# Kernel tuning notes

Hardware: AMD Instinct MI355X
Metric: run time of the kernel (lower is better)

Reference implementation:

```python
import jax, jax.numpy as jnp
import numpy as np

STRIDES = (8, 16, 32, 64, 128)
NUM_CONVS = 4
GROUPS = 32
EPS = 1e-5
FEAT_SHAPES = [(8, 256, 100, 152), (8, 256, 50, 76), (8, 256, 25, 38), (8, 256, 13, 19), (8, 256, 7, 10)]


def _conv3x3(x, w, b):
    # x: [B,C,H,W], w: [O,I,3,3] -> SAME padding, stride 1
    y = jax.lax.conv_general_dilated(x, w, (1, 1), 'SAME', dimension_numbers=('NCHW', 'OIHW', 'NCHW'))
    return y + b[None, :, None, None]


def _group_norm(x, g, b):
    B, C, H, W = x.shape
    xr = x.reshape(B, GROUPS, C // GROUPS, H, W)
    m = xr.mean(axis=(2, 3, 4), keepdims=True)
    v = xr.var(axis=(2, 3, 4), keepdims=True)
    xr = (xr - m) * jax.lax.rsqrt(v + EPS)
    return xr.reshape(B, C, H, W) * g[None, :, None, None] + b[None, :, None, None]


def _head(feats, cls_w, cls_b, cls_gn_g, cls_gn_b, box_w, box_b, box_gn_g, box_gn_b,
          logits_w, logits_b, ctr_w, ctr_b, reg_w, reg_b, scales):
    outs = []
    for l, f in enumerate(feats):
        ct, bt = f, f
        for i in range(NUM_CONVS):  # fixed-depth tower loop
            ct = jax.nn.relu(_group_norm(_conv3x3(ct, cls_w[i], cls_b[i]), cls_gn_g[i], cls_gn_b[i]))
            bt = jax.nn.relu(_group_norm(_conv3x3(bt, box_w[i], box_b[i]), box_gn_g[i], box_gn_b[i]))
        logits = _conv3x3(ct, logits_w, logits_b)          # [B,80,H,W]
        ctr = _conv3x3(ct, ctr_w, ctr_b)                   # [B,1,H,W]
        reg = jnp.exp(scales[l] * _conv3x3(bt, reg_w, reg_b))  # [B,4,H,W], torch.exp(Scale(bbox_pred))
        B = f.shape[0]
        outs.append(jnp.concatenate([logits, reg, ctr], axis=1).reshape(B, -1))
    return jnp.concatenate(outs, axis=1)  # [B, sum_l 85*H_l*W_l]


def _locations(feats):
    # FCOS grid locations: (x,y) center of each stride cell, per level, concatenated
    locs = []
    for l, f in enumerate(feats):
        h, w = f.shape[-2:]
        s = STRIDES[l]
        sx = jnp.arange(w, dtype=jnp.float32) * s + s // 2
        sy = jnp.arange(h, dtype=jnp.float32) * s + s // 2
        yy, xx = jnp.meshgrid(sy, sx, indexing='ij')
        locs.append(jnp.stack([xx.reshape(-1), yy.reshape(-1)], axis=1))
    return jnp.concatenate(locs, axis=0)  # [sum HW, 2]


def setup_inputs() -> dict:
    key = jax.random.key(0)
    ks = jax.random.split(key, 12)
    d = {}
    for i, s in enumerate(FEAT_SHAPES):
        d['feat%d' % i] = jax.random.normal(ks[i], s, dtype=jnp.float32)

    def w(k, shape):
        return jax.random.normal(k, shape, dtype=jnp.float32) * 0.01  # init std=0.01

    d['cls_w'] = w(ks[5], (NUM_CONVS, 256, 256, 3, 3))
    d['cls_b'] = jnp.zeros((NUM_CONVS, 256), jnp.float32)
    d['cls_gn_g'] = jnp.ones((NUM_CONVS, 256), jnp.float32)
    d['cls_gn_b'] = jnp.zeros((NUM_CONVS, 256), jnp.float32)
    d['box_w'] = w(ks[6], (NUM_CONVS, 256, 256, 3, 3))
    d['box_b'] = jnp.zeros((NUM_CONVS, 256), jnp.float32)
    d['box_gn_g'] = jnp.ones((NUM_CONVS, 256), jnp.float32)
    d['box_gn_b'] = jnp.zeros((NUM_CONVS, 256), jnp.float32)
    d['logits_w'] = w(ks[7], (80, 256, 3, 3))
    d['logits_b'] = jnp.full((80,), -float(np.log((1.0 - 0.01) / 0.01)), jnp.float32)  # prior_prob bias
    d['ctr_w'] = w(ks[8], (1, 256, 3, 3))
    d['ctr_b'] = jnp.zeros((1,), jnp.float32)
    d['reg_w'] = w(ks[9], (4, 256, 3, 3))
    d['reg_b'] = jnp.zeros((4,), jnp.float32)
    d['scales'] = jnp.ones((5,), jnp.float32)
    return d


def reference(feat0, feat1, feat2, feat3, feat4, cls_w, cls_b, cls_gn_g, cls_gn_b,
              box_w, box_b, box_gn_g, box_gn_b, logits_w, logits_b, ctr_w, ctr_b,
              reg_w, reg_b, scales):
    feats = [feat0, feat1, feat2, feat3, feat4]
    out = _head(feats, cls_w, cls_b, cls_gn_g, cls_gn_b, box_w, box_b, box_gn_g, box_gn_b,
                logits_w, logits_b, ctr_w, ctr_b, reg_w, reg_b, scales)
    locs = _locations(feats)
    return out, locs
```

## Files before the change

kernel.cpp:

```cpp
#include <hip/hip_runtime.h>
#include <hip/hip_bf16.h>

#define TOT85 1722695ULL

using short8 = __attribute__((ext_vector_type(8))) short;
using f32x4  = __attribute__((ext_vector_type(4))) float;

struct Feat5 { const float* p[5]; };

__device__ __forceinline__ float bfbits2f(short u) {
  return __uint_as_float(((unsigned int)(unsigned short)u) << 16);
}
__device__ __forceinline__ short f2bfbits(float f) {
  __hip_bfloat16 h = __float2bfloat16(f);
  return *reinterpret_cast<short*>(&h);
}

#define LVL_TABLES                                                              \
  constexpr int kH[5] = {100, 50, 25, 13, 7};                                   \
  constexpr int kW[5] = {152, 76, 38, 19, 10};                                  \
  constexpr int kNTx[5] = {10, 5, 3, 2, 1};                                     \
  constexpr int kCumT[5] = {0, 130, 165, 177, 181};                             \
  constexpr int kCumHW[5] = {0, 15200, 19000, 19950, 20197};                    \
  constexpr float kInv[5] = {1.f / 121600.f, 1.f / 30400.f, 1.f / 7600.f,       \
                             1.f / 1976.f, 1.f / 560.f};

__global__ __launch_bounds__(256) void repack_k(const float* __restrict__ src,
                                                __hip_bfloat16* __restrict__ dst,
                                                int O, int NOCP, int ocoff) {
  int idx = blockIdx.x * 256 + threadIdx.x;
  if (idx >= O * 2304) return;
  int o = idx / 2304;
  int r = idx - o * 2304;
  int i = r / 9;
  int t = r - i * 9;
  dst[((size_t)(t * 8 + (i >> 5)) * NOCP + (o + ocoff)) * 32 + (i & 31)] =
      __float2bfloat16(src[idx]);
}

__global__ void locations_all_k(float* __restrict__ out) {
  LVL_TABLES
  constexpr int kStride[5] = {8, 16, 32, 64, 128};
  int i = blockIdx.x * 256 + threadIdx.x;
  if (i >= 20267) return;
  int lvl = (i >= 15200) + (i >= 19000) + (i >= 19950) + (i >= 20197);
  int local = i - kCumHW[lvl];
  int W = kW[lvl];
  float s = (float)kStride[lvl];
  int y = local / W, x = local - y * W;
  out[2 * i + 0] = x * s + 0.5f * s;
  out[2 * i + 1] = y * s + 0.5f * s;
}

template <bool NORM_IN, bool SRC_NCHW>
__global__ __launch_bounds__(256, 2) void conv_tower_k(
    Feat5 feats, const __hip_bfloat16* __restrict__ srcb_base,
    const __hip_bfloat16* __restrict__ wpk, const float* __restrict__ bias,
    const float* __restrict__ statsInBase, const float* __restrict__ gamma,
    const float* __restrict__ beta, __hip_bfloat16* __restrict__ dstBase,
    float* __restrict__ statsOutBase) {
  LVL_TABLES
  __shared__ __align__(16) short s_in[180 * 40];
  __shared__ float s_red[64];
  __shared__ float s_a[256], s_c[256];

  const int tid = threadIdx.x;
  const int lane = tid & 63;
  const int wave = tid >> 6;
  const int wm = wave >> 1;
  const int wn = wave & 1;
  const int bx = blockIdx.x;
  const int lvl = (bx >= 130) + (bx >= 165) + (bx >= 177) + (bx >= 181);
  const int H = kH[lvl], W = kW[lvl], nTx = kNTx[lvl];
  const int tloc = bx - kCumT[lvl];
  const int ty = tloc / nTx, tx = tloc - ty * nTx;
  const int x0 = tx * 16, y0 = ty * 8;
  const int b = blockIdx.z;
  const int HW = H * W;
  const size_t lbase = (size_t)2048 * kCumHW[lvl];
  const int l15 = lane & 15;
  const int kg = lane >> 4;
  const int q8 = (tid & 3) * 8;

  if (tid < 64) s_red[tid] = 0.f;
  if (NORM_IN) {
    const float* statsIn = statsInBase + (size_t)lvl * 4096;
    float inv_cnt = kInv[lvl];
    int g = tid >> 3;
    float s = statsIn[(b * 32 + g) * 2 + 0];
    float ss = statsIn[(b * 32 + g) * 2 + 1];
    float m = s * inv_cnt;
    float var = fmaf(-m, m, ss * inv_cnt);
    float rs = rsqrtf(var + 1e-5f);
    float avv = rs * gamma[tid];
    s_a[tid] = avv;
    s_c[tid] = fmaf(-m, avv, beta[tid]);
  }

  f32x4 acc[4][8];
#pragma unroll
  for (int m = 0; m < 4; ++m)
#pragma unroll
    for (int n = 0; n < 8; ++n) acc[m][n] = (f32x4){0.f, 0.f, 0.f, 0.f};

  const short* wlane = (const short*)wpk + ((wn * 128 + l15) * 32 + kg * 8);
  const size_t TAPSTR = (size_t)8 * 256 * 32;

  for (int chunk = 0; chunk < 8; ++chunk) {
    const int ic0 = chunk * 32;
    __syncthreads();
    if (SRC_NCHW) {
      const float* srcf = feats.p[lvl];
      const int pix = tid;
      if (pix < 180) {
        int prow = pix / 18;
        int pcol = pix - prow * 18;
        int gy = y0 + prow - 1, gx = x0 + pcol - 1;
        short8 sv[4];
        bool valid = (gy >= 0 && gy < H && gx >= 0 && gx < W);
        if (valid) {
          const float* p = srcf + (((size_t)(b * 256 + ic0)) * H + gy) * W + gx;
#pragma unroll
          for (int q = 0; q < 4; ++q)
#pragma unroll
            for (int j = 0; j < 8; ++j)
              sv[q][j] = f2bfbits(p[(size_t)(q * 8 + j) * HW]);
        } else {
#pragma unroll
          for (int q = 0; q < 4; ++q) sv[q] = (short8)0;
        }
#pragma unroll
        for (int q = 0; q < 4; ++q) *(short8*)(s_in + pix * 40 + q * 8) = sv[q];
      }
    } else {
      const short* srcb = (const short*)srcb_base + lbase;
      float av[8], cv[8];
#pragma unroll
      for (int j = 0; j < 8; ++j) {
        int c2 = ic0 + q8 + j;
        av[j] = s_a[c2];
        cv[j] = s_c[c2];
      }
      for (int idx = tid; idx < 720; idx += 256) {
        int pix = idx >> 2;
        int prow = pix / 18;
        int pcol = pix - prow * 18;
        int gy = y0 + prow - 1, gx = x0 + pcol - 1;
        short8 o8 = (short8)0;
        if (gy >= 0 && gy < H && gx >= 0 && gx < W) {
          const short* sp = srcb + ((((size_t)b * H + gy) * W + gx) * 256 + ic0 + q8);
          short8 v8 = *(const short8*)sp;
#pragma unroll
          for (int j = 0; j < 8; ++j)
            o8[j] = f2bfbits(fmaxf(fmaf(bfbits2f(v8[j]), av[j], cv[j]), 0.f));
        }
        *(short8*)(s_in + pix * 40 + q8) = o8;
      }
    }
    __syncthreads();

    const short* wch = wlane + (size_t)chunk * 256 * 32;
    short8 bwA[8], bwB[8];
#pragma unroll
    for (int n = 0; n < 8; ++n) bwA[n] = *(const short8*)(wch + n * 512);

    auto tapbody = [&](int tap, short8* curw, short8* nxtw) {
      if (tap < 8) {
        const short* wt = wch + (size_t)(tap + 1) * TAPSTR;
#pragma unroll
        for (int n = 0; n < 8; ++n) nxtw[n] = *(const short8*)(wt + n * 512);
      }
      const int dy = tap / 3, dx = tap - dy * 3;
      short8 af[4];
#pragma unroll
      for (int m = 0; m < 4; ++m)
        af[m] = *(const short8*)(s_in + ((wm * 4 + m + dy) * 18 + (l15 + dx)) * 40 + kg * 8);
#pragma unroll
      for (int m = 0; m < 4; ++m)
#pragma unroll
        for (int n = 0; n < 8; ++n)
          acc[m][n] = __builtin_amdgcn_mfma_f32_16x16x32_bf16(af[m], curw[n], acc[m][n], 0, 0, 0);
    };
#pragma unroll
    for (int tap = 0; tap < 9; tap += 2) {
      tapbody(tap, bwA, bwB);
      if (tap + 1 < 9) tapbody(tap + 1, bwB, bwA);
    }
  }

  short* dst = (short*)dstBase + lbase;
  const int masks[5] = {1, 2, 4, 16, 32};
#pragma unroll
  for (int n = 0; n < 8; ++n) {
    int oc_g = wn * 128 + n * 16 + l15;
    float bv = bias[oc_g];
    float lsum = 0.f, lssq = 0.f;
#pragma unroll
    for (int m = 0; m < 4; ++m) {
      int oy = y0 + wm * 4 + m;
#pragma unroll
      for (int r = 0; r < 4; ++r) {
        int ox = x0 + kg * 4 + r;
        bool valid = (oy < H) && (ox < W);
        float v = acc[m][n][r] + bv;
        if (valid) {
          dst[(((size_t)b * H + oy) * W + ox) * 256 + oc_g] = f2bfbits(v);
          lsum += v;
          lssq += v * v;
        }
      }
    }
#pragma unroll
    for (int s = 0; s < 5; ++s) {
      lsum += __shfl_xor(lsum, masks[s], 64);
      lssq += __shfl_xor(lssq, masks[s], 64);
    }
    if ((lane & 55) == 0) {
      int g2 = ((wn * 8 + n) * 2 + ((lane >> 3) & 1)) * 2;
      atomicAdd(&s_red[g2 + 0], lsum);
      atomicAdd(&s_red[g2 + 1], lssq);
    }
  }
  __syncthreads();
  float* statsOut = statsOutBase + (size_t)lvl * 4096;
  if (tid < 64) atomicAdd(&statsOut[(size_t)b * 64 + tid], s_red[tid]);
}

template <int NREP, int OUT_MODE>
__global__ __launch_bounds__(256, 3) void conv_head_k(
    const __hip_bfloat16* __restrict__ srcb_base, const __hip_bfloat16* __restrict__ wpk,
    const float* __restrict__ bias, const float* __restrict__ bias2,
    const float* __restrict__ statsInBase, const float* __restrict__ gamma,
    const float* __restrict__ beta, float* __restrict__ out,
    const float* __restrict__ scales, int NOCP) {
  LVL_TABLES
  __shared__ __align__(16) short s_in[180 * 40];
  __shared__ float s_a[256], s_c[256];

  const int tid = threadIdx.x;
  const int lane = tid & 63;
  const int wave = tid >> 6;
  const int wm = wave >> 1;
  const int wn = wave & 1;
  const int bx = blockIdx.x;
  const int lvl = (bx >= 130) + (bx >= 165) + (bx >= 177) + (bx >= 181);
  const int H = kH[lvl], W = kW[lvl], nTx = kNTx[lvl];
  const int tloc = bx - kCumT[lvl];
  const int ty = tloc / nTx, tx = tloc - ty * nTx;
  const int x0 = tx * 16, y0 = ty * 8;
  const int b = blockIdx.z;
  const int HW = H * W;
  const size_t lbase = (size_t)2048 * kCumHW[lvl];
  float* out_lvl = out + (size_t)85 * kCumHW[lvl];
  const int l15 = lane & 15;
  const int kg = lane >> 4;
  const int q8 = (tid & 3) * 8;

  {
    const float* statsIn = statsInBase + (size_t)lvl * 4096;
    float inv_cnt = kInv[lvl];
    int g = tid >> 3;
    float s = statsIn[(b * 32 + g) * 2 + 0];
    float ss = statsIn[(b * 32 + g) * 2 + 1];
    float m = s * inv_cnt;
    float var = fmaf(-m, m, ss * inv_cnt);
    float rs = rsqrtf(var + 1e-5f);
    float avv = rs * gamma[tid];
    s_a[tid] = avv;
    s_c[tid] = fmaf(-m, avv, beta[tid]);
  }

  f32x4 acc[4][NREP];
#pragma unroll
  for (int m = 0; m < 4; ++m)
#pragma unroll
    for (int n = 0; n < NREP; ++n) acc[m][n] = (f32x4){0.f, 0.f, 0.f, 0.f};

  const short* wlane = (const short*)wpk + ((wn * NREP * 16 + l15) * 32 + kg * 8);
  const size_t TAPSTR = (size_t)8 * NOCP * 32;

  for (int chunk = 0; chunk < 8; ++chunk) {
    const int ic0 = chunk * 32;
    __syncthreads();
    {
      const short* srcb = (const short*)srcb_base + lbase;
      float av[8], cv[8];
#pragma unroll
      for (int j = 0; j < 8; ++j) {
        int c2 = ic0 + q8 + j;
        av[j] = s_a[c2];
        cv[j] = s_c[c2];
      }
      for (int idx = tid; idx < 720; idx += 256) {
        int pix = idx >> 2;
        int prow = pix / 18;
        int pcol = pix - prow * 18;
        int gy = y0 + prow - 1, gx = x0 + pcol - 1;
        short8 o8 = (short8)0;
        if (gy >= 0 && gy < H && gx >= 0 && gx < W) {
          const short* sp = srcb + ((((size_t)b * H + gy) * W + gx) * 256 + ic0 + q8);
          short8 v8 = *(const short8*)sp;
#pragma unroll
          for (int j = 0; j < 8; ++j)
            o8[j] = f2bfbits(fmaxf(fmaf(bfbits2f(v8[j]), av[j], cv[j]), 0.f));
        }
        *(short8*)(s_in + pix * 40 + q8) = o8;
      }
    }
    __syncthreads();

    const short* wch = wlane + (size_t)chunk * NOCP * 32;
    short8 bwA[NREP], bwB[NREP];
#pragma unroll
    for (int n = 0; n < NREP; ++n) bwA[n] = *(const short8*)(wch + n * 512);

    auto tapbody = [&](int tap, short8* curw, short8* nxtw) {
      if (tap < 8) {
        const short* wt = wch + (size_t)(tap + 1) * TAPSTR;
#pragma unroll
        for (int n = 0; n < NREP; ++n) nxtw[n] = *(const short8*)(wt + n * 512);
      }
      const int dy = tap / 3, dx = tap - dy * 3;
      short8 af[4];
#pragma unroll
      for (int m = 0; m < 4; ++m)
        af[m] = *(const short8*)(s_in + ((wm * 4 + m + dy) * 18 + (l15 + dx)) * 40 + kg * 8);
#pragma unroll
      for (int m = 0; m < 4; ++m)
#pragma unroll
        for (int n = 0; n < NREP; ++n)
          acc[m][n] = __builtin_amdgcn_mfma_f32_16x16x32_bf16(af[m], curw[n], acc[m][n], 0, 0, 0);
    };
#pragma unroll
    for (int tap = 0; tap < 9; tap += 2) {
      tapbody(tap, bwA, bwB);
      if (tap + 1 < 9) tapbody(tap + 1, bwB, bwA);
    }
  }

#pragma unroll
  for (int n = 0; n < NREP; ++n) {
    int oc_l = wn * NREP * 16 + n * 16 + l15;
    int oc_valid = (OUT_MODE == 1) ? 81 : 4;
    float bv;
    if (OUT_MODE == 1)
      bv = (oc_l < 80) ? bias[oc_l] : ((oc_l == 80) ? bias2[0] : 0.f);
    else
      bv = (oc_l < oc_valid) ? bias[oc_l] : 0.f;
#pragma unroll
    for (int m = 0; m < 4; ++m) {
      int oy = y0 + wm * 4 + m;
#pragma unroll
      for (int r = 0; r < 4; ++r) {
        int ox = x0 + kg * 4 + r;
        bool valid = (oy < H) && (ox < W) && (oc_l < oc_valid);
        float v = acc[m][n][r] + bv;
        if (valid) {
          if (OUT_MODE == 1) {
            int och = (oc_l == 80) ? 84 : oc_l;
            out_lvl[(size_t)b * TOT85 + (size_t)och * HW + oy * W + ox] = v;
          } else {
            out_lvl[(size_t)b * TOT85 + (size_t)(80 + oc_l) * HW + oy * W + ox] =
                expf(scales[lvl] * v);
          }
        }
      }
    }
  }
}

extern "C" void kernel_launch(void* const* d_in, const int* in_sizes, int n_in,
                              void* d_out_v, int out_size, void* d_ws, size_t ws_size,
                              hipStream_t stream) {
  (void)in_sizes; (void)n_in; (void)out_size; (void)ws_size;

  Feat5 feats;
  for (int i = 0; i < 5; ++i) feats.p[i] = (const float*)d_in[i];
  Feat5 featsNull;
  for (int i = 0; i < 5; ++i) featsNull.p[i] = nullptr;
  const float* cls_w = (const float*)d_in[5];
  const float* cls_b = (const float*)d_in[6];
  const float* cls_g = (const float*)d_in[7];
  const float* cls_bb = (const float*)d_in[8];
  const float* box_w = (const float*)d_in[9];
  const float* box_b = (const float*)d_in[10];
  const float* box_g = (const float*)d_in[11];
  const float* box_bb = (const float*)d_in[12];
  const float* logits_w = (const float*)d_in[13];
  const float* logits_b = (const float*)d_in[14];
  const float* ctr_w = (const float*)d_in[15];
  const float* ctr_b = (const float*)d_in[16];
  const float* reg_w = (const float*)d_in[17];
  const float* reg_b = (const float*)d_in[18];
  const float* scales = (const float*)d_in[19];
  float* d_out = (float*)d_out_v;

  char* wsp = (char*)d_ws;
  size_t off = 0;
  auto carve = [&](size_t bytes) -> char* {
    char* p = wsp + off;
    off += (bytes + 255) & ~(size_t)255;
    return p;
  };
  const size_t ALLE = (size_t)8 * 20267 * 256;
  __hip_bfloat16* bufA = (__hip_bfloat16*)carve(ALLE * 2);
  __hip_bfloat16* bufB = (__hip_bfloat16*)carve(ALLE * 2);
  const size_t TW = (size_t)9 * 8 * 256 * 32;
  __hip_bfloat16* wpk_cls = (__hip_bfloat16*)carve(4 * TW * 2);
  __hip_bfloat16* wpk_box = (__hip_bfloat16*)carve(4 * TW * 2);
  __hip_bfloat16* wpk_clsh = (__hip_bfloat16*)carve((size_t)9 * 8 * 96 * 32 * 2);
  __hip_bfloat16* wpk_regh = (__hip_bfloat16*)carve((size_t)9 * 8 * 32 * 32 * 2);
  float* stats_all = (float*)carve((size_t)40 * 512 * 4);

  hipMemsetAsync(stats_all, 0, (size_t)40 * 512 * 4, stream);

  auto rp = [&](const float* s, __hip_bfloat16* d, int O, int NOCP, int ocoff) {
    int total = O * 2304;
    hipLaunchKernelGGL(repack_k, dim3((total + 255) / 256), dim3(256), 0, stream, s, d, O, NOCP,
                       ocoff);
  };
  for (int i = 0; i < 4; ++i) {
    rp(cls_w + (size_t)i * 256 * 2304, wpk_cls + (size_t)i * TW, 256, 256, 0);
    rp(box_w + (size_t)i * 256 * 2304, wpk_box + (size_t)i * TW, 256, 256, 0);
  }
  rp(logits_w, wpk_clsh, 80, 96, 0);
  rp(ctr_w, wpk_clsh, 1, 96, 80);
  rp(reg_w, wpk_regh, 4, 32, 0);

  const size_t OUT0 = (size_t)8 * TOT85;
  hipLaunchKernelGGL(locations_all_k, dim3(80), dim3(256), 0, stream, d_out + OUT0);

  dim3 grid(182, 1, 8);
  dim3 blk(256);

  for (int t = 0; t < 2; ++t) {
    const __hip_bfloat16* wpkT = (t == 0) ? wpk_cls : wpk_box;
    const float* bt = (t == 0) ? cls_b : box_b;
    const float* gt = (t == 0) ? cls_g : box_g;
    const float* bbt = (t == 0) ? cls_bb : box_bb;
    auto slot = [&](int i) { return stats_all + (size_t)(t * 4 + i) * 512; };

    hipLaunchKernelGGL((conv_tower_k<false, true>), grid, blk, 0, stream, feats,
                       (const __hip_bfloat16*)nullptr, wpkT, bt, (const float*)nullptr,
                       (const float*)nullptr, (const float*)nullptr, bufA, slot(0));
    __hip_bfloat16* cur = bufA;
    __hip_bfloat16* nxt = bufB;
    for (int i = 1; i < 4; ++i) {
      hipLaunchKernelGGL((conv_tower_k<true, false>), grid, blk, 0, stream, featsNull,
                         (const __hip_bfloat16*)cur, wpkT + (size_t)i * TW, bt + i * 256,
                         slot(i - 1), gt + (i - 1) * 256, bbt + (i - 1) * 256, nxt, slot(i));
      __hip_bfloat16* tmp = cur;
      cur = nxt;
      nxt = tmp;
    }
    if (t == 0) {
      hipLaunchKernelGGL((conv_head_k<3, 1>), grid, blk, 0, stream, (const __hip_bfloat16*)cur,
                         wpk_clsh, logits_b, ctr_b, slot(3), gt + 3 * 256, bbt + 3 * 256,
                         d_out, scales, 96);
    } else {
      hipLaunchKernelGGL((conv_head_k<1, 2>), grid, blk, 0, stream, (const __hip_bfloat16*)cur,
                         wpk_regh, reg_b, (const float*)nullptr, slot(3), gt + 3 * 256,
                         bbt + 3 * 256, d_out, scales, 32);
    }
  }
}
```

Measured before the change: 2.488 ms.

## Widen conv input chunks to 64 channels and prefetch global loads before barrier

The conv tower kernel now stages 64 input channels per shared-memory chunk instead of 32, halving the number of chunk iterations and their barriers. Global loads for the next tile are issued into registers before the __syncthreads, so memory latency can overlap with waves still finishing MFMA work on the previous chunk. The inner loop runs 18 k-steps (9 taps × 2 sub-chunks) with weight double-buffering. This costs more LDS (180×72 shorts) and more registers (fv[32], pv[6]), which may reduce occupancy under launch_bounds(256,2).

```diff
diff --git a/kernel.cpp b/kernel.cpp
--- a/kernel.cpp
+++ b/kernel.cpp
@@ -60,7 +60,7 @@
     const float* __restrict__ beta, __hip_bfloat16* __restrict__ dstBase,
     float* __restrict__ statsOutBase) {
   LVL_TABLES
-  __shared__ __align__(16) short s_in[180 * 40];
+  __shared__ __align__(16) short s_in[180 * 72];
   __shared__ float s_red[64];
   __shared__ float s_a[256], s_c[256];
 
@@ -80,7 +80,7 @@
   const size_t lbase = (size_t)2048 * kCumHW[lvl];
   const int l15 = lane & 15;
   const int kg = lane >> 4;
-  const int q8 = (tid & 3) * 8;
+  const int q8x = (tid & 7) * 8;
 
   if (tid < 64) s_red[tid] = 0.f;
   if (NORM_IN) {
@@ -104,77 +104,119 @@
     for (int n = 0; n < 8; ++n) acc[m][n] = (f32x4){0.f, 0.f, 0.f, 0.f};
 
   const short* wlane = (const short*)wpk + ((wn * 128 + l15) * 32 + kg * 8);
-  const size_t TAPSTR = (size_t)8 * 256 * 32;
-
-  for (int chunk = 0; chunk < 8; ++chunk) {
-    const int ic0 = chunk * 32;
-    __syncthreads();
+
+  const int pixN = tid;
+  int prowN = pixN / 18;
+  int pcolN = pixN - prowN * 18;
+  const int gyN = y0 + prowN - 1, gxN = x0 + pcolN - 1;
+  const bool validN = (pixN < 180) && (gyN >= 0 && gyN < H && gxN >= 0 && gxN < W);
+
+  for (int c = 0; c < 4; ++c) {
+    const int ic0 = c * 64;
+
+    short8 pv[6];
+    float fv[32];
     if (SRC_NCHW) {
       const float* srcf = feats.p[lvl];
-      const int pix = tid;
-      if (pix < 180) {
-        int prow = pix / 18;
-        int pcol = pix - prow * 18;
-        int gy = y0 + prow - 1, gx = x0 + pcol - 1;
-        short8 sv[4];
-        bool valid = (gy >= 0 && gy < H && gx >= 0 && gx < W);
-        if (valid) {
-          const float* p = srcf + (((size_t)(b * 256 + ic0)) * H + gy) * W + gx;
-#pragma unroll
-          for (int q = 0; q < 4; ++q)
-#pragma unroll
-            for (int j = 0; j < 8; ++j)
-              sv[q][j] = f2bfbits(p[(size_t)(q * 8 + j) * HW]);
-        } else {
-#pragma unroll
-          for (int q = 0; q < 4; ++q) sv[q] = (short8)0;
-        }
-#pragma unroll
-        for (int q = 0; q < 4; ++q) *(short8*)(s_in + pix * 40 + q * 8) = sv[q];
+      if (validN) {
+        const float* p = srcf + (((size_t)(b * 256 + ic0)) * H + gyN) * W + gxN;
+#pragma unroll
+        for (int j = 0; j < 32; ++j) fv[j] = p[(size_t)j * HW];
       }
     } else {
       const short* srcb = (const short*)srcb_base + lbase;
+#pragma unroll
+      for (int r = 0; r < 6; ++r) {
+        int idx = r * 256 + tid;
+        pv[r] = (short8)0;
+        if (idx < 1440) {
+          int px = idx >> 3;
+          int prow = px / 18;
+          int pcol = px - prow * 18;
+          int gy = y0 + prow - 1, gx = x0 + pcol - 1;
+          if (gy >= 0 && gy < H && gx >= 0 && gx < W)
+            pv[r] = *(const short8*)(srcb +
+                                     ((((size_t)b * H + gy) * W + gx) * 256 + ic0 + q8x));
+        }
+      }
+    }
+
+    __syncthreads();
+
+    if (SRC_NCHW) {
+      const float* srcf = feats.p[lvl];
+      if (pixN < 180) {
+        short8 sv[4];
+        if (validN) {
+#pragma unroll
+          for (int q = 0; q < 4; ++q)
+#pragma unroll
+            for (int j = 0; j < 8; ++j) sv[q][j] = f2bfbits(fv[q * 8 + j]);
+        } else {
+#pragma unroll
+          for (int q = 0; q < 4; ++q) sv[q] = (short8)0;
+        }
+#pragma unroll
+        for (int q = 0; q < 4; ++q) *(short8*)(s_in + pixN * 72 + q * 8) = sv[q];
+        if (validN) {
+          const float* p = srcf + (((size_t)(b * 256 + ic0 + 32)) * H + gyN) * W + gxN;
+#pragma unroll
+          for (int j = 0; j < 32; ++j) fv[j] = p[(size_t)j * HW];
+#pragma unroll
+          for (int q = 0; q < 4; ++q)
+#pragma unroll
+            for (int j = 0; j < 8; ++j) sv[q][j] = f2bfbits(fv[q * 8 + j]);
+        }
+#pragma unroll
+        for (int q = 0; q < 4; ++q) *(short8*)(s_in + pixN * 72 + 32 + q * 8) = sv[q];
+      }
+    } else {
       float av[8], cv[8];
 #pragma unroll
       for (int j = 0; j < 8; ++j) {
-        int c2 = ic0 + q8 + j;
+        int c2 = ic0 + q8x + j;
         av[j] = s_a[c2];
         cv[j] = s_c[c2];
       }
-      for (int idx = tid; idx < 720; idx += 256) {
-        int pix = idx >> 2;
-        int prow = pix / 18;
-        int pcol = pix - prow * 18;
-        int gy = y0 + prow - 1, gx = x0 + pcol - 1;
-        short8 o8 = (short8)0;
-        if (gy >= 0 && gy < H && gx >= 0 && gx < W) {
-          const short* sp = srcb + ((((size_t)b * H + gy) * W + gx) * 256 + ic0 + q8);
-          short8 v8 = *(const short8*)sp;
-#pragma unroll
-          for (int j = 0; j < 8; ++j)
-            o8[j] = f2bfbits(fmaxf(fmaf(bfbits2f(v8[j]), av[j], cv[j]), 0.f));
-        }
-        *(short8*)(s_in + pix * 40 + q8) = o8;
+#pragma unroll
+      for (int r = 0; r < 6; ++r) {
+        int idx = r * 256 + tid;
+        if (idx < 1440) {
+          int px = idx >> 3;
+          int prow = px / 18;
+          int pcol = px - prow * 18;
+          int gy = y0 + prow - 1, gx = x0 + pcol - 1;
+          short8 o8 = (short8)0;
+          if (gy >= 0 && gy < H && gx >= 0 && gx < W) {
+#pragma unroll
+            for (int j = 0; j < 8; ++j)
+              o8[j] = f2bfbits(fmaxf(fmaf(bfbits2f(pv[r][j]), av[j], cv[j]), 0.f));
+          }
+          *(short8*)(s_in + px * 72 + q8x) = o8;
+        }
       }
     }
     __syncthreads();
 
-    const short* wch = wlane + (size_t)chunk * 256 * 32;
+    const short* wcb = wlane + (size_t)c * 2 * 8192;
     short8 bwA[8], bwB[8];
 #pragma unroll
-    for (int n = 0; n < 8; ++n) bwA[n] = *(const short8*)(wch + n * 512);
-
-    auto tapbody = [&](int tap, short8* curw, short8* nxtw) {
-      if (tap < 8) {
-        const short* wt = wch + (size_t)(tap + 1) * TAPSTR;
+    for (int n = 0; n < 8; ++n) bwA[n] = *(const short8*)(wcb + n * 512);
+
+    auto kbody = [&](int k, short8* curw, short8* nxtw) {
+      if (k < 17) {
+        int kn = k + 1;
+        const short* wt = wcb + ((size_t)((kn >> 1) * 8 + (kn & 1))) * 8192;
 #pragma unroll
         for (int n = 0; n < 8; ++n) nxtw[n] = *(const short8*)(wt + n * 512);
       }
+      const int tap = k >> 1, sub = k & 1;
       const int dy = tap / 3, dx = tap - dy * 3;
       short8 af[4];
 #pragma unroll
       for (int m = 0; m < 4; ++m)
-        af[m] = *(const short8*)(s_in + ((wm * 4 + m + dy) * 18 + (l15 + dx)) * 40 + kg * 8);
+        af[m] = *(const short8*)(s_in + ((wm * 4 + m + dy) * 18 + (l15 + dx)) * 72 +
+                                 sub * 32 + kg * 8);
 #pragma unroll
       for (int m = 0; m < 4; ++m)
 #pragma unroll
@@ -182,9 +224,9 @@
           acc[m][n] = __builtin_amdgcn_mfma_f32_16x16x32_bf16(af[m], curw[n], acc[m][n], 0, 0, 0);
     };
 #pragma unroll
-    for (int tap = 0; tap < 9; tap += 2) {
-      tapbody(tap, bwA, bwB);
-      if (tap + 1 < 9) tapbody(tap + 1, bwB, bwA);
+    for (int k = 0; k < 18; k += 2) {
+      kbody(k, bwA, bwB);
+      kbody(k + 1, bwB, bwA);
     }
   }
 
```

Result: no change. 2.446 ms (-1.7%).

## Stage conv weights in LDS via direct loads and retile tower conv to 32x8x128

Applied to the files above, without the earlier changes.

The tower conv kernel now uses 512-thread blocks covering a 32-wide by 8-tall pixel tile and half of the output channels, with the grid split over output-channel halves. Each 32-channel chunk of the weight panel is copied into shared memory with global_load_lds, replacing per-lane register streaming of weights from global memory, and the padded layout is meant to reduce LDS bank conflicts. Input activations for the next chunk are loaded into registers before the barrier to overlap global latency. The cost is much more LDS per block (about 100KB), which may limit occupancy, and input halos are reloaded once per output-channel half.

```diff
diff --git a/kernel.cpp b/kernel.cpp
--- a/kernel.cpp
+++ b/kernel.cpp
@@ -14,6 +14,11 @@
 __device__ __forceinline__ short f2bfbits(float f) {
   __hip_bfloat16 h = __float2bfloat16(f);
   return *reinterpret_cast<short*>(&h);
+}
+__device__ __forceinline__ void gload_lds16(const void* g, void* l) {
+  __builtin_amdgcn_global_load_lds(
+      (const __attribute__((address_space(1))) unsigned int*)g,
+      (__attribute__((address_space(3))) unsigned int*)l, 16, 0, 0);
 }
 
 #define LVL_TABLES                                                              \
@@ -21,6 +26,14 @@
   constexpr int kW[5] = {152, 76, 38, 19, 10};                                  \
   constexpr int kNTx[5] = {10, 5, 3, 2, 1};                                     \
   constexpr int kCumT[5] = {0, 130, 165, 177, 181};                             \
+  constexpr int kCumHW[5] = {0, 15200, 19000, 19950, 20197};                    \
+  constexpr float kInv[5] = {1.f / 121600.f, 1.f / 30400.f, 1.f / 7600.f,       \
+                             1.f / 1976.f, 1.f / 560.f};
+#define LVL_TABLES32                                                            \
+  constexpr int kH[5] = {100, 50, 25, 13, 7};                                   \
+  constexpr int kW[5] = {152, 76, 38, 19, 10};                                  \
+  constexpr int kNTx32[5] = {5, 3, 2, 1, 1};                                    \
+  constexpr int kCumT32[5] = {0, 65, 86, 94, 96};                               \
   constexpr int kCumHW[5] = {0, 15200, 19000, 19950, 20197};                    \
   constexpr float kInv[5] = {1.f / 121600.f, 1.f / 30400.f, 1.f / 7600.f,       \
                              1.f / 1976.f, 1.f / 560.f};
@@ -35,6 +48,18 @@
   int i = r / 9;
   int t = r - i * 9;
   dst[((size_t)(t * 8 + (i >> 5)) * NOCP + (o + ocoff)) * 32 + (i & 31)] =
+      __float2bfloat16(src[idx]);
+}
+
+__global__ __launch_bounds__(256) void repack_big_k(const float* __restrict__ src,
+                                                    __hip_bfloat16* __restrict__ dst) {
+  int idx = blockIdx.x * 256 + threadIdx.x;
+  if (idx >= 256 * 2304) return;
+  int o = idx / 2304;
+  int r = idx - o * 2304;
+  int i = r / 9;
+  int t = r - i * 9;
+  dst[((((size_t)(o >> 7) * 8 + (i >> 5)) * 9 + t) * 128 + (o & 127)) * 40 + (i & 31)] =
       __float2bfloat16(src[idx]);
 }
 
@@ -53,37 +78,40 @@
 }
 
 template <bool NORM_IN, bool SRC_NCHW>
-__global__ __launch_bounds__(256, 2) void conv_tower_k(
+__global__ __launch_bounds__(512, 2) void conv_tower_k(
     Feat5 feats, const __hip_bfloat16* __restrict__ srcb_base,
     const __hip_bfloat16* __restrict__ wpk, const float* __restrict__ bias,
     const float* __restrict__ statsInBase, const float* __restrict__ gamma,
     const float* __restrict__ beta, __hip_bfloat16* __restrict__ dstBase,
     float* __restrict__ statsOutBase) {
-  LVL_TABLES
-  __shared__ __align__(16) short s_in[180 * 40];
-  __shared__ float s_red[64];
+  LVL_TABLES32
+  __shared__ __align__(16) short s_in[340 * 40];
+  __shared__ __align__(16) short s_w[9 * 128 * 40];
+  __shared__ float s_red[32];
   __shared__ float s_a[256], s_c[256];
 
   const int tid = threadIdx.x;
   const int lane = tid & 63;
   const int wave = tid >> 6;
-  const int wm = wave >> 1;
   const int wn = wave & 1;
+  const int wm = (wave >> 1) & 1;
+  const int wq = wave >> 2;
   const int bx = blockIdx.x;
-  const int lvl = (bx >= 130) + (bx >= 165) + (bx >= 177) + (bx >= 181);
-  const int H = kH[lvl], W = kW[lvl], nTx = kNTx[lvl];
-  const int tloc = bx - kCumT[lvl];
+  const int lvl = (bx >= 65) + (bx >= 86) + (bx >= 94) + (bx >= 96);
+  const int H = kH[lvl], W = kW[lvl], nTx = kNTx32[lvl];
+  const int tloc = bx - kCumT32[lvl];
   const int ty = tloc / nTx, tx = tloc - ty * nTx;
-  const int x0 = tx * 16, y0 = ty * 8;
+  const int x0 = tx * 32, y0 = ty * 8;
   const int b = blockIdx.z;
+  const int ochalf = blockIdx.y;
   const int HW = H * W;
   const size_t lbase = (size_t)2048 * kCumHW[lvl];
   const int l15 = lane & 15;
   const int kg = lane >> 4;
   const int q8 = (tid & 3) * 8;
 
-  if (tid < 64) s_red[tid] = 0.f;
-  if (NORM_IN) {
+  if (tid < 32) s_red[tid] = 0.f;
+  if (NORM_IN && tid < 256) {
     const float* statsIn = statsInBase + (size_t)lvl * 4096;
     float inv_cnt = kInv[lvl];
     int g = tid >> 3;
@@ -97,24 +125,51 @@
     s_c[tid] = fmaf(-m, avv, beta[tid]);
   }
 
-  f32x4 acc[4][8];
+  f32x4 acc[4][4];
 #pragma unroll
   for (int m = 0; m < 4; ++m)
 #pragma unroll
-    for (int n = 0; n < 8; ++n) acc[m][n] = (f32x4){0.f, 0.f, 0.f, 0.f};
-
-  const short* wlane = (const short*)wpk + ((wn * 128 + l15) * 32 + kg * 8);
-  const size_t TAPSTR = (size_t)8 * 256 * 32;
+    for (int n = 0; n < 4; ++n) acc[m][n] = (f32x4){0.f, 0.f, 0.f, 0.f};
+
+  const short* wpanel = (const short*)wpk + (size_t)ochalf * (8 * 9 * 128 * 40);
 
   for (int chunk = 0; chunk < 8; ++chunk) {
     const int ic0 = chunk * 32;
+
+    short8 pv[3];
+    if (!SRC_NCHW) {
+      const short* srcb = (const short*)srcb_base + lbase;
+#pragma unroll
+      for (int r = 0; r < 3; ++r) {
+        int idx = r * 512 + tid;
+        pv[r] = (short8)0;
+        if (idx < 1360) {
+          int px = idx >> 2;
+          int prow = px / 34, pcol = px - prow * 34;
+          int gy = y0 + prow - 1, gx = x0 + pcol - 1;
+          if (gy >= 0 && gy < H && gx >= 0 && gx < W)
+            pv[r] = *(const short8*)(srcb +
+                                     ((((size_t)b * H + gy) * W + gx) * 256 + ic0 + q8));
+        }
+      }
+    }
+
     __syncthreads();
+
+    {
+      const short* wsrc = wpanel + (size_t)chunk * (9 * 128 * 40);
+#pragma unroll
+      for (int r = 0; r < 12; ++r) {
+        int u = r * 512 + tid;
+        if (u < 5760)
+          gload_lds16(wsrc + (size_t)u * 8, s_w + (size_t)(r * 512 + wave * 64) * 8);
+      }
+    }
+
     if (SRC_NCHW) {
       const float* srcf = feats.p[lvl];
-      const int pix = tid;
-      if (pix < 180) {
-        int prow = pix / 18;
-        int pcol = pix - prow * 18;
+      if (tid < 340) {
+        int prow = tid / 34, pcol = tid - prow * 34;
         int gy = y0 + prow - 1, gx = x0 + pcol - 1;
         short8 sv[4];
         bool valid = (gy >= 0 && gy < H && gx >= 0 && gx < W);
@@ -130,10 +185,9 @@
           for (int q = 0; q < 4; ++q) sv[q] = (short8)0;
         }
 #pragma unroll
-        for (int q = 0; q < 4; ++q) *(short8*)(s_in + pix * 40 + q * 8) = sv[q];
+        for (int q = 0; q < 4; ++q) *(short8*)(s_in + tid * 40 + q * 8) = sv[q];
       }
     } else {
-      const short* srcb = (const short*)srcb_base + lbase;
       float av[8], cv[8];
 #pragma unroll
       for (int j = 0; j < 8; ++j) {
@@ -141,58 +195,50 @@
         av[j] = s_a[c2];
         cv[j] = s_c[c2];
       }
-      for (int idx = tid; idx < 720; idx += 256) {
-        int pix = idx >> 2;
-        int prow = pix / 18;
-        int pcol = pix - prow * 18;
-        int gy = y0 + prow - 1, gx = x0 + pcol - 1;
-        short8 o8 = (short8)0;
-        if (gy >= 0 && gy < H && gx >= 0 && gx < W) {
-          const short* sp = srcb + ((((size_t)b * H + gy) * W + gx) * 256 + ic0 + q8);
-          short8 v8 = *(const short8*)sp;
-#pragma unroll
-          for (int j = 0; j < 8; ++j)
-            o8[j] = f2bfbits(fmaxf(fmaf(bfbits2f(v8[j]), av[j], cv[j]), 0.f));
+#pragma unroll
+      for (int r = 0; r < 3; ++r) {
+        int idx = r * 512 + tid;
+        if (idx < 1360) {
+          int px = idx >> 2;
+          int prow = px / 34, pcol = px - prow * 34;
+          int gy = y0 + prow - 1, gx = x0 + pcol - 1;
+          short8 o8 = (short8)0;
+          if (gy >= 0 && gy < H && gx >= 0 && gx < W) {
+#pragma unroll
+            for (int j = 0; j < 8; ++j)
+              o8[j] = f2bfbits(fmaxf(fmaf(bfbits2f(pv[r][j]), av[j], cv[j]), 0.f));
+          }
+          *(short8*)(s_in + px * 40 + q8) = o8;
         }
-        *(short8*)(s_in + pix * 40 + q8) = o8;
       }
     }
     __syncthreads();
 
-    const short* wch = wlane + (size_t)chunk * 256 * 32;
-    short8 bwA[8], bwB[8];
-#pragma unroll
-    for (int n = 0; n < 8; ++n) bwA[n] = *(const short8*)(wch + n * 512);
-
-    auto tapbody = [&](int tap, short8* curw, short8* nxtw) {
-      if (tap < 8) {
-        const short* wt = wch + (size_t)(tap + 1) * TAPSTR;
-#pragma unroll
-        for (int n = 0; n < 8; ++n) nxtw[n] = *(const short8*)(wt + n * 512);
-      }
+#pragma unroll
+    for (int tap = 0; tap < 9; ++tap) {
       const int dy = tap / 3, dx = tap - dy * 3;
+      short8 wf[4];
+#pragma unroll
+      for (int n = 0; n < 4; ++n)
+        wf[n] = *(const short8*)(s_w + ((tap * 128 + wn * 64 + n * 16 + l15) * 40 + kg * 8));
       short8 af[4];
 #pragma unroll
       for (int m = 0; m < 4; ++m)
-        af[m] = *(const short8*)(s_in + ((wm * 4 + m + dy) * 18 + (l15 + dx)) * 40 + kg * 8);
+        af[m] = *(const short8*)(s_in +
+                                 (((wm * 4 + m + dy) * 34 + (wq * 16 + l15 + dx)) * 40 + kg * 8));
 #pragma unroll
       for (int m = 0; m < 4; ++m)
 #pragma unroll
-        for (int n = 0; n < 8; ++n)
-          acc[m][n] = __builtin_amdgcn_mfma_f32_16x16x32_bf16(af[m], curw[n], acc[m][n], 0, 0, 0);
-    };
-#pragma unroll
-    for (int tap = 0; tap < 9; tap += 2) {
-      tapbody(tap, bwA, bwB);
-      if (tap + 1 < 9) tapbody(tap + 1, bwB, bwA);
+        for (int n = 0; n < 4; ++n)
+          acc[m][n] = __builtin_amdgcn_mfma_f32_16x16x32_bf16(af[m], wf[n], acc[m][n], 0, 0, 0);
     }
   }
 
   short* dst = (short*)dstBase + lbase;
   const int masks[5] = {1, 2, 4, 16, 32};
 #pragma unroll
-  for (int n = 0; n < 8; ++n) {
-    int oc_g = wn * 128 + n * 16 + l15;
+  for (int n = 0; n < 4; ++n) {
+    int oc_g = ochalf * 128 + wn * 64 + n * 16 + l15;
     float bv = bias[oc_g];
     float lsum = 0.f, lssq = 0.f;
 #pragma unroll
@@ -200,7 +246,7 @@
       int oy = y0 + wm * 4 + m;
 #pragma unroll
       for (int r = 0; r < 4; ++r) {
-        int ox = x0 + kg * 4 + r;
+        int ox = x0 + wq * 16 + kg * 4 + r;
         bool valid = (oy < H) && (ox < W);
         float v = acc[m][n][r] + bv;
         if (valid) {
@@ -216,14 +262,14 @@
       lssq += __shfl_xor(lssq, masks[s], 64);
     }
     if ((lane & 55) == 0) {
-      int g2 = ((wn * 8 + n) * 2 + ((lane >> 3) & 1)) * 2;
+      int g2 = (wn * 8 + n * 2 + ((lane >> 3) & 1)) * 2;
       atomicAdd(&s_red[g2 + 0], lsum);
       atomicAdd(&s_red[g2 + 1], lssq);
     }
   }
   __syncthreads();
   float* statsOut = statsOutBase + (size_t)lvl * 4096;
-  if (tid < 64) atomicAdd(&statsOut[(size_t)b * 64 + tid], s_red[tid]);
+  if (tid < 32) atomicAdd(&statsOut[(size_t)b * 64 + ochalf * 32 + tid], s_red[tid]);
 }
 
 template <int NREP, int OUT_MODE>
@@ -405,9 +451,9 @@
   const size_t ALLE = (size_t)8 * 20267 * 256;
   __hip_bfloat16* bufA = (__hip_bfloat16*)carve(ALLE * 2);
   __hip_bfloat16* bufB = (__hip_bfloat16*)carve(ALLE * 2);
-  const size_t TW = (size_t)9 * 8 * 256 * 32;
-  __hip_bfloat16* wpk_cls = (__hip_bfloat16*)carve(4 * TW * 2);
-  __hip_bfloat16* wpk_box = (__hip_bfloat16*)carve(4 * TW * 2);
+  const size_t TWB = (size_t)2 * 8 * 9 * 128 * 40;
+  __hip_bfloat16* big_cls = (__hip_bfloat16*)carve(4 * TWB * 2);
+  __hip_bfloat16* big_box = (__hip_bfloat16*)carve(4 * TWB * 2);
   __hip_bfloat16* wpk_clsh = (__hip_bfloat16*)carve((size_t)9 * 8 * 96 * 32 * 2);
   __hip_bfloat16* wpk_regh = (__hip_bfloat16*)carve((size_t)9 * 8 * 32 * 32 * 2);
   float* stats_all = (float*)carve((size_t)40 * 512 * 4);
@@ -420,8 +466,10 @@
                        ocoff);
   };
   for (int i = 0; i < 4; ++i) {
-    rp(cls_w + (size_t)i * 256 * 2304, wpk_cls + (size_t)i * TW, 256, 256, 0);
-    rp(box_w + (size_t)i * 256 * 2304, wpk_box + (size_t)i * TW, 256, 256, 0);
+    hipLaunchKernelGGL(repack_big_k, dim3(2304), dim3(256), 0, stream,
+                       cls_w + (size_t)i * 256 * 2304, big_cls + (size_t)i * TWB);
+    hipLaunchKernelGGL(repack_big_k, dim3(2304), dim3(256), 0, stream,
+                       box_w + (size_t)i * 256 * 2304, big_box + (size_t)i * TWB);
   }
   rp(logits_w, wpk_clsh, 80, 96, 0);
   rp(ctr_w, wpk_clsh, 1, 96, 80);
@@ -430,37 +478,38 @@
   const size_t OUT0 = (size_t)8 * TOT85;
   hipLaunchKernelGGL(locations_all_k, dim3(80), dim3(256), 0, stream, d_out + OUT0);
 
-  dim3 grid(182, 1, 8);
-  dim3 blk(256);
+  dim3 gridT(97, 2, 8);
+  dim3 gridH(182, 1, 8);
+  dim3 blkT(512), blkH(256);
 
   for (int t = 0; t < 2; ++t) {
-    const __hip_bfloat16* wpkT = (t == 0) ? wpk_cls : wpk_box;
+    const __hip_bfloat16* bigT = (t == 0) ? big_cls : big_box;
     const float* bt = (t == 0) ? cls_b : box_b;
     const float* gt = (t == 0) ? cls_g : box_g;
     const float* bbt = (t == 0) ? cls_bb : box_bb;
     auto slot = [&](int i) { return stats_all + (size_t)(t * 4 + i) * 512; };
 
-    hipLaunchKernelGGL((conv_tower_k<false, true>), grid, blk, 0, stream, feats,
-                       (const __hip_bfloat16*)nullptr, wpkT, bt, (const float*)nullptr,
+    hipLaunchKernelGGL((conv_tower_k<false, true>), gridT, blkT, 0, stream, feats,
+                       (const __hip_bfloat16*)nullptr, bigT, bt, (const float*)nullptr,
                        (const float*)nullptr, (const float*)nullptr, bufA, slot(0));
     __hip_bfloat16* cur = bufA;
     __hip_bfloat16* nxt = bufB;
     for (int i = 1; i < 4; ++i) {
-      hipLaunchKernelGGL((conv_tower_k<true, false>), grid, blk, 0, stream, featsNull,
-                         (const __hip_bfloat16*)cur, wpkT + (size_t)i * TW, bt + i * 256,
+      hipLaunchKernelGGL((conv_tower_k<true, false>), gridT, blkT, 0, stream, featsNull,
+                         (const __hip_bfloat16*)cur, bigT + (size_t)i * TWB, bt + i * 256,
                          slot(i - 1), gt + (i - 1) * 256, bbt + (i - 1) * 256, nxt, slot(i));
       __hip_bfloat16* tmp = cur;
       cur = nxt;
       nxt = tmp;
     }
     if (t == 0) {
-      hipLaunchKernelGGL((conv_head_k<3, 1>), grid, blk, 0, stream, (const __hip_bfloat16*)cur,
-                         wpk_clsh, logits_b, ctr_b, slot(3), gt + 3 * 256, bbt + 3 * 256,
-                         d_out, scales, 96);
+      hipLaunchKernelGGL((conv_head_k<3, 1>), gridH, blkH, 0, stream,
+                         (const __hip_bfloat16*)cur, wpk_clsh, logits_b, ctr_b, slot(3),
+                         gt + 3 * 256, bbt + 3 * 256, d_out, scales, 96);
     } else {
-      hipLaunchKernelGGL((conv_head_k<1, 2>), grid, blk, 0, stream, (const __hip_bfloat16*)cur,
-                         wpk_regh, reg_b, (const float*)nullptr, slot(3), gt + 3 * 256,
-                         bbt + 3 * 256, d_out, scales, 32);
-    }
-  }
-}
+      hipLaunchKernelGGL((conv_head_k<1, 2>), gridH, blkH, 0, stream,
+                         (const __hip_bfloat16*)cur, wpk_regh, reg_b, (const float*)nullptr,
+                         slot(3), gt + 3 * 256, bbt + 3 * 256, d_out, scales, 32);
+    }
+  }
+}
```

After: 2.571 ms. 3.3% more time.
